# Performance work log

Measured on AMD Instinct MI355X. Metric: run time of the kernel, lower is better.

Reference implementation:

```python
import jax, jax.numpy as jnp
import numpy as np

B, N, DK, DM = 8, 4096, 512, 64

def setup_inputs() -> dict:
    key = jax.random.key(0)
    ks = jax.random.split(key, 7)
    K = jax.random.normal(ks[0], (B, N, DK), dtype=jnp.float32)
    Q = jax.random.normal(ks[1], (B, N, DK), dtype=jnp.float32)
    V = jax.random.normal(ks[2], (B, N, DK), dtype=jnp.float32)
    s = 1.0 / np.sqrt(DK)
    Wk = jax.random.normal(ks[3], (DM, DK), dtype=jnp.float32) * s
    bk = jax.random.normal(ks[4], (DM,), dtype=jnp.float32) * 0.01
    Wq = jax.random.normal(ks[5], (DM, DK), dtype=jnp.float32) * s
    bq = jax.random.normal(ks[6], (DM,), dtype=jnp.float32) * 0.01
    return {"K": K, "Q": Q, "V": V, "Wk": Wk, "bk": bk, "Wq": Wq, "bq": bq}

def reference(K, Q, V, Wk, bk, Wq, bq):
    # Linear projections (torch Linear: x @ W.T + b)
    pk = jnp.einsum('bnd,md->bnm', K, Wk) + bk  # [B,N,DM]
    pq = jnp.einsum('bnd,md->bnm', Q, Wq) + bq  # [B,M,DM]
    scale = 1.0 / np.sqrt(DM).astype(np.float32)
    scores = jnp.einsum('bqm,bkm->bqk', pq, pk) * scale  # [B,M,N]
    attn = jax.nn.softmax(scores, axis=-1)
    return jnp.einsum('bqk,bkd->bqd', attn, V)  # V unprojected, as in original
```

## Files before the change

### kernel.cpp

```cpp
#include <hip/hip_runtime.h>
#include <hip/hip_bf16.h>
#include <cstdint>


#define DEVINL __device__ __forceinline__

using f32x4  = __attribute__((ext_vector_type(4)))  float;
using bf16x8 = __attribute__((ext_vector_type(8)))  short;
using bf16x4 = __attribute__((ext_vector_type(4)))  short;

constexpr int BATCH = 8;
constexpr int N     = 4096;
constexpr int DK    = 512;
constexpr int DM    = 64;
constexpr int KVB   = 64;
constexpr int QB    = 128;
constexpr int STEPS = N / KVB;

#define PQ_SCALE 0.18033688011112042f
#define FM 10.0f

DEVINL short cvt_bf16(float x) {
  uint32_t u = __float_as_uint(x);
  uint32_t r = u + 0x7fffu + ((u >> 16) & 1u);
  return (short)(r >> 16);
}

DEVINL uint32_t cvtpk(float lo, float hi) {
  uint32_t r;
  asm("v_cvt_pk_bf16_f32 %0, %1, %2" : "=v"(r) : "v"(lo), "v"(hi));
  return r;
}

DEVINL void async16(void* lds, const void* g) {
  __builtin_amdgcn_global_load_lds(
      (const __attribute__((address_space(1))) uint32_t*)(uintptr_t)g,
      (__attribute__((address_space(3))) uint32_t*)(uint32_t)(uintptr_t)lds,
      16, 0, 0);
}

DEVINL f32x4 mfma16(bf16x8 a, bf16x8 b, f32x4 c) {
  return __builtin_amdgcn_mfma_f32_16x16x32_bf16(a, b, c, 0, 0, 0);
}

#define LGKM0_BAR() do { \
  asm volatile("s_waitcnt lgkmcnt(0)" ::: "memory"); \
  __builtin_amdgcn_s_barrier(); \
} while (0)

__global__ __launch_bounds__(256) void wconv_kernel(
    const float* __restrict__ Wk, const float* __restrict__ Wq,
    short* __restrict__ WkB, short* __restrict__ WqB) {
  int i = blockIdx.x * 256 + threadIdx.x;
  WkB[i] = cvt_bf16(Wk[i]);
  WqB[i] = cvt_bf16(Wq[i]);
}

__global__ __launch_bounds__(256) void vtrans_kernel(
    const float* __restrict__ V, short* __restrict__ Vt) {
  int bb = blockIdx.x;
  int b  = bb >> 9;
  int nt = (bb >> 3) & 63;
  int dt = bb & 7;
  int n0 = nt * 64, d0 = dt * 64;
  __shared__ short t_lds[64][80];
  int tid = threadIdx.x;
#pragma unroll
  for (int it = 0; it < 4; ++it) {
    int idx = it * 256 + tid;
    int row = idx >> 4;
    int c4  = idx & 15;
    f32x4 v = *(const f32x4*)&V[((size_t)b * N + n0 + row) * DK + d0 + c4 * 4];
#pragma unroll
    for (int j = 0; j < 4; ++j) t_lds[c4 * 4 + j][row] = cvt_bf16(v[j]);
  }
  __syncthreads();
#pragma unroll
  for (int it = 0; it < 2; ++it) {
    int idx = it * 256 + tid;
    int rd = idx >> 3;
    int ck = idx & 7;
    bf16x8 vv = *(const bf16x8*)&t_lds[rd][ck * 8];
    *(bf16x8*)&Vt[((size_t)b * DK + d0 + rd) * N + n0 + ck * 8] = vv;
  }
}

__global__ __launch_bounds__(512, 2) void proj_kernel(
    const float* __restrict__ Q, const float* __restrict__ K,
    const short* __restrict__ WqB, const short* __restrict__ WkB,
    const float* __restrict__ bq, const float* __restrict__ bk,
    short* __restrict__ pq, short* __restrict__ pk) {
  bool isK = blockIdx.x >= 256;
  const float* X    = isK ? K : Q;
  const short* W    = isK ? WkB : WqB;
  const float* bias = isK ? bk : bq;
  short* P          = isK ? pk : pq;
  float sc          = isK ? 1.0f : PQ_SCALE;
  int rb = (blockIdx.x & 255) * 128;

  __shared__ short x_lds[128 * 512];
  int tid = threadIdx.x, w = tid >> 6, lane = tid & 63, g = lane >> 4, c = lane & 15;

#pragma unroll
  for (int it = 0; it < 32; ++it) {
    int idx4 = it * 512 + tid;
    int row  = idx4 >> 7;
    int col  = (idx4 & 127) * 4;
    f32x4 v = *(const f32x4*)&X[((size_t)rb + row) * DK + col];
    bf16x4 hb;
#pragma unroll
    for (int j = 0; j < 4; ++j) hb[j] = cvt_bf16(v[j]);
    int scz = (col >> 3) ^ (row & 7);
    *(bf16x4*)&x_lds[row * 512 + scz * 8 + ((col >> 2) & 1) * 4] = hb;
  }
  __syncthreads();

  f32x4 o[4];
#pragma unroll
  for (int mt = 0; mt < 4; ++mt) o[mt] = f32x4{0.f, 0.f, 0.f, 0.f};
  int arow = w * 16 + c;
#pragma unroll
  for (int ks = 0; ks < 16; ++ks) {
    int scz = (ks * 4 + g) ^ (arow & 7);
    bf16x8 a = *(const bf16x8*)&x_lds[arow * 512 + scz * 8];
#pragma unroll
    for (int mt = 0; mt < 4; ++mt) {
      bf16x8 bfr = *(const bf16x8*)&W[(size_t)(mt * 16 + c) * DK + ks * 32 + g * 8];
      o[mt] = mfma16(a, bfr, o[mt]);
    }
  }
#pragma unroll
  for (int mt = 0; mt < 4; ++mt) {
    float bb = bias[mt * 16 + c];
#pragma unroll
    for (int r = 0; r < 4; ++r) {
      int row = rb + w * 16 + g * 4 + r;
      P[(size_t)row * DM + mt * 16 + c] = cvt_bf16((o[mt][r] + bb) * sc);
    }
  }
}

__global__ __launch_bounds__(1024, 4) void flash_kernel(
    const short* __restrict__ pq, const short* __restrict__ pk,
    const short* __restrict__ vt, float* __restrict__ out) {
  int b  = blockIdx.x & 7;
  int qt = blockIdx.x >> 3;
  int q0 = qt * QB;

  int tid = threadIdx.x, w = tid >> 6, lane = tid & 63, g = lane >> 4, c = lane & 15;
  int cs = c & 7;
  int qg = w & 7, kqh = w >> 3;
  int qrow = qg * 16 + c;
  int vh = w >> 3, vs = w & 7;

  __shared__ short vt_lds[2][DK * KVB];
  __shared__ short pk_lds[KVB * DM];
  __shared__ short p_lds[QB * KVB];
  __shared__ float lsum2[2][QB];

  const short* pkr0 = pk_lds + (kqh * 32 + c) * 64 + ((g ^ cs) * 8);
  const short* pkr1 = pk_lds + (kqh * 32 + c) * 64 + (((4 + g) ^ cs) * 8);
  short* pw0 = p_lds + qrow * 64 + (((kqh * 4 + 0 + (g >> 1)) ^ cs) * 8) + (g & 1) * 4;
  short* pw1 = p_lds + qrow * 64 + (((kqh * 4 + 2 + (g >> 1)) ^ cs) * 8) + (g & 1) * 4;

  const short* pfr0 = p_lds + (vh * 64 + c) * 64 + ((g ^ cs) * 8);
  const short* pfr1 = p_lds + (vh * 64 + c) * 64 + (((4 + g) ^ cs) * 8);
  const short* vfA0 = &vt_lds[0][(vs * 64 + c) * 64 + ((g ^ cs) * 8)];
  const short* vfA1 = &vt_lds[0][(vs * 64 + c) * 64 + (((4 + g) ^ cs) * 8)];
  const short* vfB0 = vfA0 + DK * KVB;
  const short* vfB1 = vfA1 + DK * KVB;

  const short* vt_base = vt + (size_t)b * DK * N;
  int tr = tid >> 3, tc = tid & 7;
  int vt_vo[4];
#pragma unroll
  for (int r = 0; r < 4; ++r)
    vt_vo[r] = (r * 128 + tr) * N + ((tc ^ (tr & 7)) * 8);
  short* vt_dst0 = &vt_lds[0][w * 512];
  short* vt_dst1 = &vt_lds[1][w * 512];

  const short* pk_base = pk + (size_t)b * N * DM;
  {
    int prow = tid >> 4, h = tid & 15;
    pk_base += prow * 64 + (((h >> 1) ^ (prow & 7)) * 8) + (h & 1) * 4;
  }
  short* pk_wr = pk_lds + tid * 4;
  bf16x4 pkreg;

  const short* pq_row = pq + ((size_t)b * N + q0 + qrow) * DM;
  bf16x8 qf0 = *(const bf16x8*)(pq_row + g * 8);
  bf16x8 qf1 = *(const bf16x8*)(pq_row + 32 + g * 8);

  f32x4 acc[4][4];
#pragma unroll
  for (int i = 0; i < 4; ++i)
#pragma unroll
    for (int j = 0; j < 4; ++j) acc[i][j] = f32x4{0.f, 0.f, 0.f, 0.f};

  float lp = 0.f;
  uint32_t pbu[4];

#pragma unroll
  for (int r = 0; r < 4; ++r)
    async16((void*)(vt_dst0 + r * 8192), (const void*)(vt_base + vt_vo[r]));
  vt_base += KVB;
  pkreg = *(const bf16x4*)pk_base;
  pk_base += KVB * DM;
  *(bf16x4*)pk_wr = pkreg;
  __syncthreads();

#pragma unroll
  for (int s = 0; s < 2; ++s) {
    bf16x8 a0 = *(const bf16x8*)(pkr0 + s * 1024);
    bf16x8 a1 = *(const bf16x8*)(pkr1 + s * 1024);
    f32x4 d = f32x4{-FM, -FM, -FM, -FM};
    d = mfma16(a0, qf0, d);
    d = mfma16(a1, qf1, d);
    float p0 = exp2f(d[0]), p1 = exp2f(d[1]);
    float p2 = exp2f(d[2]), p3 = exp2f(d[3]);
    lp += (p0 + p1) + (p2 + p3);
    pbu[s * 2]     = cvtpk(p0, p1);
    pbu[s * 2 + 1] = cvtpk(p2, p3);
  }
  pkreg = *(const bf16x4*)pk_base;
  pk_base += KVB * DM;
  LGKM0_BAR();
  *(uint2*)pw0 = uint2{pbu[0], pbu[1]};
  *(uint2*)pw1 = uint2{pbu[2], pbu[3]};
  *(bf16x4*)pk_wr = pkreg;
  LGKM0_BAR();
  __builtin_amdgcn_sched_barrier(0);

  for (int t = 0; t < STEPS - 1; ++t) {
    int vb = t & 1;
    pkreg = *(const bf16x4*)pk_base;
    pk_base += KVB * DM;
    __builtin_amdgcn_sched_barrier(0);
    short* vdst = vb ? vt_dst0 : vt_dst1;
#pragma unroll
    for (int r = 0; r < 4; ++r)
      async16((void*)(vdst + r * 8192), (const void*)(vt_base + vt_vo[r]));
    vt_base += KVB;
    asm volatile("s_waitcnt vmcnt(5)" ::: "memory");
    __builtin_amdgcn_sched_barrier(0);

#pragma unroll
    for (int s = 0; s < 2; ++s) {
      bf16x8 a0 = *(const bf16x8*)(pkr0 + s * 1024);
      bf16x8 a1 = *(const bf16x8*)(pkr1 + s * 1024);
      f32x4 d = f32x4{-FM, -FM, -FM, -FM};
      d = mfma16(a0, qf0, d);
      d = mfma16(a1, qf1, d);
      float p0 = exp2f(d[0]), p1 = exp2f(d[1]);
      float p2 = exp2f(d[2]), p3 = exp2f(d[3]);
      lp += (p0 + p1) + (p2 + p3);
      pbu[s * 2]     = cvtpk(p0, p1);
      pbu[s * 2 + 1] = cvtpk(p2, p3);
    }

    const short* vf0 = vb ? vfB0 : vfA0;
    const short* vf1 = vb ? vfB1 : vfA1;
    __builtin_amdgcn_s_setprio(1);
    {
      bf16x8 vf[4];
#pragma unroll
      for (int i = 0; i < 4; ++i) vf[i] = *(const bf16x8*)(vf0 + i * 1024);
#pragma unroll
      for (int j = 0; j < 4; ++j) {
        bf16x8 pf = *(const bf16x8*)(pfr0 + j * 1024);
#pragma unroll
        for (int i = 0; i < 4; ++i) acc[i][j] = mfma16(vf[i], pf, acc[i][j]);
      }
#pragma unroll
      for (int i = 0; i < 4; ++i) vf[i] = *(const bf16x8*)(vf1 + i * 1024);
#pragma unroll
      for (int j = 0; j < 4; ++j) {
        bf16x8 pf = *(const bf16x8*)(pfr1 + j * 1024);
#pragma unroll
        for (int i = 0; i < 4; ++i) acc[i][j] = mfma16(vf[i], pf, acc[i][j]);
      }
    }
    __builtin_amdgcn_s_setprio(0);

    LGKM0_BAR();
    __builtin_amdgcn_sched_barrier(0);

    if (t < STEPS - 2) *(bf16x4*)pk_wr = pkreg;
    *(uint2*)pw0 = uint2{pbu[0], pbu[1]};
    *(uint2*)pw1 = uint2{pbu[2], pbu[3]};
    LGKM0_BAR();
    __builtin_amdgcn_sched_barrier(0);
  }

  asm volatile("s_waitcnt vmcnt(0)" ::: "memory");
  __builtin_amdgcn_sched_barrier(0);
  {
    int vb = (STEPS - 1) & 1;
    const short* vf0 = vb ? vfB0 : vfA0;
    const short* vf1 = vb ? vfB1 : vfA1;
    bf16x8 vf[4];
#pragma unroll
    for (int i = 0; i < 4; ++i) vf[i] = *(const bf16x8*)(vf0 + i * 1024);
#pragma unroll
    for (int j = 0; j < 4; ++j) {
      bf16x8 pf = *(const bf16x8*)(pfr0 + j * 1024);
#pragma unroll
      for (int i = 0; i < 4; ++i) acc[i][j] = mfma16(vf[i], pf, acc[i][j]);
    }
#pragma unroll
    for (int i = 0; i < 4; ++i) vf[i] = *(const bf16x8*)(vf1 + i * 1024);
#pragma unroll
    for (int j = 0; j < 4; ++j) {
      bf16x8 pf = *(const bf16x8*)(pfr1 + j * 1024);
#pragma unroll
      for (int i = 0; i < 4; ++i) acc[i][j] = mfma16(vf[i], pf, acc[i][j]);
    }
  }

  lp += __shfl_xor(lp, 16);
  lp += __shfl_xor(lp, 32);
  if (g == 0) lsum2[kqh][qrow] = lp;
  LGKM0_BAR();

  float* out_b = out + (size_t)b * N * DK;
#pragma unroll
  for (int j = 0; j < 4; ++j) {
    int qq = vh * 64 + j * 16 + c;
    float rl = 1.f / (lsum2[0][qq] + lsum2[1][qq]);
    int q = q0 + qq;
#pragma unroll
    for (int i = 0; i < 4; ++i) {
      f32x4 o = acc[i][j];
      o[0] *= rl; o[1] *= rl; o[2] *= rl; o[3] *= rl;
      *(f32x4*)&out_b[(size_t)q * DK + vs * 64 + i * 16 + g * 4] = o;
    }
  }
}

extern "C" void kernel_launch(void* const* d_in, const int* in_sizes, int n_in,
                              void* d_out, int out_size, void* d_ws, size_t ws_size,
                              hipStream_t stream) {
  (void)in_sizes; (void)n_in; (void)out_size; (void)ws_size;
  const float* K  = (const float*)d_in[0];
  const float* Q  = (const float*)d_in[1];
  const float* V  = (const float*)d_in[2];
  const float* Wk = (const float*)d_in[3];
  const float* bk = (const float*)d_in[4];
  const float* Wq = (const float*)d_in[5];
  const float* bq = (const float*)d_in[6];
  float* out = (float*)d_out;

  char* ws = (char*)d_ws;
  short* pq  = (short*)(ws + 0);
  short* pk  = (short*)(ws + ((size_t)4 << 20));
  short* vt  = (short*)(ws + ((size_t)8 << 20));
  short* WqB = (short*)(ws + ((size_t)40 << 20));
  short* WkB = (short*)(ws + ((size_t)40 << 20) + 64 * 512 * 2);

  hipLaunchKernelGGL(wconv_kernel,  dim3(128),  dim3(256), 0, stream, Wk, Wq, WkB, WqB);
  hipLaunchKernelGGL(vtrans_kernel, dim3(4096), dim3(256), 0, stream, V, vt);
  hipLaunchKernelGGL(proj_kernel,   dim3(512),  dim3(512), 0, stream, Q, K, WqB, WkB, bq, bk, pq, pk);
  hipLaunchKernelGGL(flash_kernel,  dim3(256),  dim3(1024), 0, stream, pq, pk, vt, out);
}
```

Baseline: 238.9 us.

## Load PK fragments directly into registers and double-buffer the P tile

```diff
diff --git a/kernel.cpp b/kernel.cpp
--- a/kernel.cpp
+++ b/kernel.cpp
@@ -16,6 +16,7 @@
 constexpr int KVB   = 64;
 constexpr int QB    = 128;
 constexpr int STEPS = N / KVB;
+constexpr int PBUF  = QB * KVB;
 
 #define PQ_SCALE 0.18033688011112042f
 #define FM 10.0f
@@ -154,21 +155,14 @@
   int vh = w >> 3, vs = w & 7;
 
   __shared__ short vt_lds[2][DK * KVB];
-  __shared__ short pk_lds[KVB * DM];
-  __shared__ short p_lds[QB * KVB];
-  __shared__ float lsum2[2][QB];
-
-  const short* pkr0 = pk_lds + (kqh * 32 + c) * 64 + ((g ^ cs) * 8);
-  const short* pkr1 = pk_lds + (kqh * 32 + c) * 64 + (((4 + g) ^ cs) * 8);
-  short* pw0 = p_lds + qrow * 64 + (((kqh * 4 + 0 + (g >> 1)) ^ cs) * 8) + (g & 1) * 4;
-  short* pw1 = p_lds + qrow * 64 + (((kqh * 4 + 2 + (g >> 1)) ^ cs) * 8) + (g & 1) * 4;
-
-  const short* pfr0 = p_lds + (vh * 64 + c) * 64 + ((g ^ cs) * 8);
-  const short* pfr1 = p_lds + (vh * 64 + c) * 64 + (((4 + g) ^ cs) * 8);
+  __shared__ short p_lds[2][PBUF];
+
+  const short* pfr0 = &p_lds[0][(vh * 64 + c) * 64 + ((g ^ cs) * 8)];
+  const short* pfr1 = &p_lds[0][(vh * 64 + c) * 64 + (((4 + g) ^ cs) * 8)];
   const short* vfA0 = &vt_lds[0][(vs * 64 + c) * 64 + ((g ^ cs) * 8)];
   const short* vfA1 = &vt_lds[0][(vs * 64 + c) * 64 + (((4 + g) ^ cs) * 8)];
-  const short* vfB0 = vfA0 + DK * KVB;
-  const short* vfB1 = vfA1 + DK * KVB;
+  short* pw0 = &p_lds[0][qrow * 64 + (((kqh * 4 + 0 + (g >> 1)) ^ cs) * 8) + (g & 1) * 4];
+  short* pw1 = &p_lds[0][qrow * 64 + (((kqh * 4 + 2 + (g >> 1)) ^ cs) * 8) + (g & 1) * 4];
 
   const short* vt_base = vt + (size_t)b * DK * N;
   int tr = tid >> 3, tc = tid & 7;
@@ -179,13 +173,7 @@
   short* vt_dst0 = &vt_lds[0][w * 512];
   short* vt_dst1 = &vt_lds[1][w * 512];
 
-  const short* pk_base = pk + (size_t)b * N * DM;
-  {
-    int prow = tid >> 4, h = tid & 15;
-    pk_base += prow * 64 + (((h >> 1) ^ (prow & 7)) * 8) + (h & 1) * 4;
-  }
-  short* pk_wr = pk_lds + tid * 4;
-  bf16x4 pkreg;
+  const short* pk_src = pk + (size_t)b * N * DM + (size_t)(kqh * 32 + c) * DM + g * 8;
 
   const short* pq_row = pq + ((size_t)b * N + q0 + qrow) * DM;
   bf16x8 qf0 = *(const bf16x8*)(pq_row + g * 8);
@@ -199,75 +187,80 @@
 
   float lp = 0.f;
   uint32_t pbu[4];
-
+  bf16x8 pkf[4];
+
+  pkf[0] = *(const bf16x8*)(pk_src);
+  pkf[1] = *(const bf16x8*)(pk_src + 32);
+  pkf[2] = *(const bf16x8*)(pk_src + 1024);
+  pkf[3] = *(const bf16x8*)(pk_src + 1056);
+  pk_src += KVB * DM;
 #pragma unroll
   for (int r = 0; r < 4; ++r)
     async16((void*)(vt_dst0 + r * 8192), (const void*)(vt_base + vt_vo[r]));
   vt_base += KVB;
-  pkreg = *(const bf16x4*)pk_base;
-  pk_base += KVB * DM;
-  *(bf16x4*)pk_wr = pkreg;
   __syncthreads();
 
 #pragma unroll
   for (int s = 0; s < 2; ++s) {
-    bf16x8 a0 = *(const bf16x8*)(pkr0 + s * 1024);
-    bf16x8 a1 = *(const bf16x8*)(pkr1 + s * 1024);
     f32x4 d = f32x4{-FM, -FM, -FM, -FM};
-    d = mfma16(a0, qf0, d);
-    d = mfma16(a1, qf1, d);
+    d = mfma16(pkf[s * 2], qf0, d);
+    d = mfma16(pkf[s * 2 + 1], qf1, d);
     float p0 = exp2f(d[0]), p1 = exp2f(d[1]);
     float p2 = exp2f(d[2]), p3 = exp2f(d[3]);
     lp += (p0 + p1) + (p2 + p3);
     pbu[s * 2]     = cvtpk(p0, p1);
     pbu[s * 2 + 1] = cvtpk(p2, p3);
   }
-  pkreg = *(const bf16x4*)pk_base;
-  pk_base += KVB * DM;
-  LGKM0_BAR();
   *(uint2*)pw0 = uint2{pbu[0], pbu[1]};
   *(uint2*)pw1 = uint2{pbu[2], pbu[3]};
-  *(bf16x4*)pk_wr = pkreg;
+  pkf[0] = *(const bf16x8*)(pk_src);
+  pkf[1] = *(const bf16x8*)(pk_src + 32);
+  pkf[2] = *(const bf16x8*)(pk_src + 1024);
+  pkf[3] = *(const bf16x8*)(pk_src + 1056);
+  pk_src += KVB * DM;
   LGKM0_BAR();
   __builtin_amdgcn_sched_barrier(0);
 
   for (int t = 0; t < STEPS - 1; ++t) {
     int vb = t & 1;
-    pkreg = *(const bf16x4*)pk_base;
-    pk_base += KVB * DM;
-    __builtin_amdgcn_sched_barrier(0);
     short* vdst = vb ? vt_dst0 : vt_dst1;
 #pragma unroll
     for (int r = 0; r < 4; ++r)
       async16((void*)(vdst + r * 8192), (const void*)(vt_base + vt_vo[r]));
     vt_base += KVB;
-    asm volatile("s_waitcnt vmcnt(5)" ::: "memory");
     __builtin_amdgcn_sched_barrier(0);
 
 #pragma unroll
     for (int s = 0; s < 2; ++s) {
-      bf16x8 a0 = *(const bf16x8*)(pkr0 + s * 1024);
-      bf16x8 a1 = *(const bf16x8*)(pkr1 + s * 1024);
       f32x4 d = f32x4{-FM, -FM, -FM, -FM};
-      d = mfma16(a0, qf0, d);
-      d = mfma16(a1, qf1, d);
+      d = mfma16(pkf[s * 2], qf0, d);
+      d = mfma16(pkf[s * 2 + 1], qf1, d);
       float p0 = exp2f(d[0]), p1 = exp2f(d[1]);
       float p2 = exp2f(d[2]), p3 = exp2f(d[3]);
       lp += (p0 + p1) + (p2 + p3);
       pbu[s * 2]     = cvtpk(p0, p1);
       pbu[s * 2 + 1] = cvtpk(p2, p3);
     }
-
-    const short* vf0 = vb ? vfB0 : vfA0;
-    const short* vf1 = vb ? vfB1 : vfA1;
-    __builtin_amdgcn_s_setprio(1);
     {
+      int po = (vb ^ 1) * PBUF;
+      *(uint2*)(pw0 + po) = uint2{pbu[0], pbu[1]};
+      *(uint2*)(pw1 + po) = uint2{pbu[2], pbu[3]};
+    }
+
+    {
+      int po = vb * PBUF;
+      int vo = vb * (DK * KVB);
+      const short* pf0 = pfr0 + po;
+      const short* pf1 = pfr1 + po;
+      const short* vf0 = vfA0 + vo;
+      const short* vf1 = vfA1 + vo;
+      __builtin_amdgcn_s_setprio(1);
       bf16x8 vf[4];
 #pragma unroll
       for (int i = 0; i < 4; ++i) vf[i] = *(const bf16x8*)(vf0 + i * 1024);
 #pragma unroll
       for (int j = 0; j < 4; ++j) {
-        bf16x8 pf = *(const bf16x8*)(pfr0 + j * 1024);
+        bf16x8 pf = *(const bf16x8*)(pf0 + j * 1024);
 #pragma unroll
         for (int i = 0; i < 4; ++i) acc[i][j] = mfma16(vf[i], pf, acc[i][j]);
       }
@@ -275,35 +268,39 @@
       for (int i = 0; i < 4; ++i) vf[i] = *(const bf16x8*)(vf1 + i * 1024);
 #pragma unroll
       for (int j = 0; j < 4; ++j) {
-        bf16x8 pf = *(const bf16x8*)(pfr1 + j * 1024);
+        bf16x8 pf = *(const bf16x8*)(pf1 + j * 1024);
 #pragma unroll
         for (int i = 0; i < 4; ++i) acc[i][j] = mfma16(vf[i], pf, acc[i][j]);
       }
-    }
-    __builtin_amdgcn_s_setprio(0);
-
+      __builtin_amdgcn_s_setprio(0);
+    }
+
+    asm volatile("s_waitcnt vmcnt(0)" ::: "memory");
+    if (t < STEPS - 2) {
+      pkf[0] = *(const bf16x8*)(pk_src);
+      pkf[1] = *(const bf16x8*)(pk_src + 32);
+      pkf[2] = *(const bf16x8*)(pk_src + 1024);
+      pkf[3] = *(const bf16x8*)(pk_src + 1056);
+      pk_src += KVB * DM;
+    }
     LGKM0_BAR();
     __builtin_amdgcn_sched_barrier(0);
-
-    if (t < STEPS - 2) *(bf16x4*)pk_wr = pkreg;
-    *(uint2*)pw0 = uint2{pbu[0], pbu[1]};
-    *(uint2*)pw1 = uint2{pbu[2], pbu[3]};
-    LGKM0_BAR();
-    __builtin_amdgcn_sched_barrier(0);
-  }
-
-  asm volatile("s_waitcnt vmcnt(0)" ::: "memory");
-  __builtin_amdgcn_sched_barrier(0);
+  }
+
   {
     int vb = (STEPS - 1) & 1;
-    const short* vf0 = vb ? vfB0 : vfA0;
-    const short* vf1 = vb ? vfB1 : vfA1;
+    int po = vb * PBUF;
+    int vo = vb * (DK * KVB);
+    const short* pf0 = pfr0 + po;
+    const short* pf1 = pfr1 + po;
+    const short* vf0 = vfA0 + vo;
+    const short* vf1 = vfA1 + vo;
     bf16x8 vf[4];
 #pragma unroll
     for (int i = 0; i < 4; ++i) vf[i] = *(const bf16x8*)(vf0 + i * 1024);
 #pragma unroll
     for (int j = 0; j < 4; ++j) {
-      bf16x8 pf = *(const bf16x8*)(pfr0 + j * 1024);
+      bf16x8 pf = *(const bf16x8*)(pf0 + j * 1024);
 #pragma unroll
       for (int i = 0; i < 4; ++i) acc[i][j] = mfma16(vf[i], pf, acc[i][j]);
     }
@@ -311,22 +308,23 @@
     for (int i = 0; i < 4; ++i) vf[i] = *(const bf16x8*)(vf1 + i * 1024);
 #pragma unroll
     for (int j = 0; j < 4; ++j) {
-      bf16x8 pf = *(const bf16x8*)(pfr1 + j * 1024);
+      bf16x8 pf = *(const bf16x8*)(pf1 + j * 1024);
 #pragma unroll
       for (int i = 0; i < 4; ++i) acc[i][j] = mfma16(vf[i], pf, acc[i][j]);
     }
   }
 
+  float* lsum2 = (float*)&p_lds[0][0];
   lp += __shfl_xor(lp, 16);
   lp += __shfl_xor(lp, 32);
-  if (g == 0) lsum2[kqh][qrow] = lp;
+  if (g == 0) lsum2[kqh * QB + qrow] = lp;
   LGKM0_BAR();
 
   float* out_b = out + (size_t)b * N * DK;
 #pragma unroll
   for (int j = 0; j < 4; ++j) {
     int qq = vh * 64 + j * 16 + c;
-    float rl = 1.f / (lsum2[0][qq] + lsum2[1][qq]);
+    float rl = 1.f / (lsum2[qq] + lsum2[QB + qq]);
     int q = q0 + qq;
 #pragma unroll
     for (int i = 0; i < 4; ++i) {
```

New measurement: 276.4 us. 1.16x slower.
